# Performance work log

Hardware: AMD Instinct MI355X
Metric: run time of the kernel (lower is better)

Reference implementation:

```python
import jax, jax.numpy as jnp
import numpy as np
from jax import lax

B, C, H, W = 4, 256, 128, 128
K = 3
EPS = 1e-5
SLOPE = 0.01  # nn.LeakyReLU default

def rpad(x, p):
    return jnp.pad(x, ((0, 0), (0, 0), (p, p), (p, p)), mode='reflect')

def conv(x, w, groups=1):
    return lax.conv_general_dilated(x, w, (1, 1), 'VALID',
        dimension_numbers=('NCHW', 'OIHW', 'NCHW'), feature_group_count=groups)

def instance_norm(x):
    m = x.mean(axis=(2, 3), keepdims=True)
    v = x.var(axis=(2, 3), keepdims=True)
    return (x - m) * lax.rsqrt(v + EPS)

def kernel_predict(s, sw, sb, pw, pb, bw, bb):
    # s: [B, SC, K, K]; reflect-padded 'same' conv keeps KxK spatial
    ws = conv(rpad(s, (K - 1) // 2), sw) + sb[None, :, None, None]
    w_spatial = ws.reshape(s.shape[0], C, 1, K, K)   # n_groups == C -> in//groups == 1
    pooled = s.mean(axis=(2, 3))                     # AdaptiveAvgPool2d((1,1))
    w_point = pooled @ pw.reshape(C, -1).T + pb      # [B, C] (1x1 grouped, groups==C)
    bias = pooled @ bw.reshape(C, -1).T + bb         # [B, C]
    return w_spatial, w_point, bias

def ada_conv(x, w_spatial, w_point, bias, cw, cb):
    x = instance_norm(x)
    xp = rpad(x, (K - 1) // 2)
    dw = lambda xi, wi: conv(xi[None], wi, groups=C)[0]
    y = jax.vmap(dw)(xp, w_spatial)                  # per-sample dynamic depthwise conv
    # grouped 1x1 conv with groups == channels == per-channel scale + bias
    y = y * w_point[:, :, None, None] + bias[:, :, None, None]
    y = conv(rpad(y, 1), cw) + cb[None, :, None, None]  # shared 3x3 reflect conv
    return y

def lrelu(x):
    return jnp.where(x >= 0, x, SLOPE * x)

def upsample2(x):
    return jnp.repeat(jnp.repeat(x, 2, axis=2), 2, axis=3)  # nn.Upsample nearest x2

def avgpool2(x):
    b, c, h, w = x.shape
    return x.reshape(b, c, h // 2, 2, w // 2, 2).mean(axis=(3, 5))


def setup_inputs() -> dict:
    key = jax.random.key(0)
    ks = jax.random.split(key, 24)
    n = lambda k, shp, s=1.0: jax.random.normal(k, shp, dtype=jnp.float32) * s
    return {
        'c_hf': n(ks[0], (B, C, H, W)),
        'c_lf': n(ks[1], (B, C, H // 2, W // 2)),
        's_hf': n(ks[2], (B, C, K, K)),
        's_lf': n(ks[3], (B, C, K, K)),
        'h_sw': n(ks[4], (C, C, K, K), 0.05), 'h_sb': n(ks[5], (C,), 0.05),
        'h_pw': n(ks[6], (C, C, 1, 1), 0.05), 'h_pb': n(ks[7], (C,), 0.05),
        'h_bw': n(ks[8], (C, C, 1, 1), 0.05), 'h_bb': n(ks[9], (C,), 0.05),
        'l_sw': n(ks[10], (C, C, K, K), 0.05), 'l_sb': n(ks[11], (C,), 0.05),
        'l_pw': n(ks[12], (C, C, 1, 1), 0.05), 'l_pb': n(ks[13], (C,), 0.05),
        'l_bw': n(ks[14], (C, C, 1, 1), 0.05), 'l_bb': n(ks[15], (C,), 0.05),
        'ada_h_w': n(ks[16], (C, C, 3, 3), 0.05), 'ada_h_b': n(ks[17], (C,), 0.05),
        'ada_l_w': n(ks[18], (C, C, 3, 3), 0.05), 'ada_l_b': n(ks[19], (C,), 0.05),
        'h2h': n(ks[20], (C, C, 3, 3), 0.05),
        'l2h': n(ks[21], (C, C, 3, 3), 0.05),
        'h2l': n(ks[22], (C, C, 3, 3), 0.05),
        'l2l': n(ks[23], (C, C, 3, 3), 0.05),
    }


def reference(c_hf, c_lf, s_hf, s_lf,
              h_sw, h_sb, h_pw, h_pb, h_bw, h_bb,
              l_sw, l_sb, l_pw, l_pb, l_bw, l_bb,
              ada_h_w, ada_h_b, ada_l_w, ada_l_b,
              h2h, l2h, h2l, l2l):
    hws, hwp, hb = kernel_predict(s_hf, h_sw, h_sb, h_pw, h_pb, h_bw, h_bb)
    lws, lwp, lb = kernel_predict(s_lf, l_sw, l_sb, l_pw, l_pb, l_bw, l_bb)
    hf = lrelu(ada_conv(c_hf, hws, hwp, hb, ada_h_w, ada_h_b))
    lf = lrelu(ada_conv(c_lf, lws, lwp, lb, ada_l_w, ada_l_b))
    # OctConv 'normal', groups=1 (not depthwise): cross-frequency fusion
    hf_out = conv(rpad(hf, 1), h2h) + conv(rpad(upsample2(lf), 1), l2h)
    lf_out = conv(rpad(lf, 1), l2l) + conv(rpad(avgpool2(hf), 1), h2l)
    return lrelu(hf_out), lrelu(lf_out)
```

## Files before the change

### kernel.cpp

```cpp
#include <hip/hip_runtime.h>
#include <hip/hip_bf16.h>

#define CDIM 256
#define EPS 1e-5f
#define SLOPE 0.01f

using f32x4  = __attribute__((ext_vector_type(4))) float;
typedef __bf16 bf16x8 __attribute__((ext_vector_type(8)));
typedef unsigned short u16x8 __attribute__((ext_vector_type(8)));

enum : size_t {
  OFF_WS_HF   = 0,
  OFF_WS_LF   = 9216,
  OFF_WP_HF   = 20480,
  OFF_BS_HF   = 21504,
  OFF_WP_LF   = 22528,
  OFF_BS_LF   = 23552,
  OFF_MEAN_HF = 24576,
  OFF_RSTD_HF = 25600,
  OFF_MEAN_LF = 26624,
  OFF_RSTD_LF = 27648,
  OFF_U16     = 32768,
};
enum : size_t {
  U_YH  = 0,
  U_YL  = 16777216,
  U_HFA = 20971520,
  U_LFA = 37748736,
  U_HFP = 41943040,
  U_PK  = 46137344,
  PK_SZ = 589824,
  U_PKPH = U_PK + 6 * PK_SZ,
  PH_SZ  = 1048576,
  U_PHB  = U_PKPH + PH_SZ,
  U_END  = U_PHB + 16777216,
};
enum : size_t { TOTAL_F = OFF_U16 + (U_END + 1) / 2 };

__device__ float g_scratch[TOTAL_F];

__device__ __forceinline__ int refl(int q, int n) {
  return q < 0 ? -q : (q >= n ? 2 * n - 2 - q : q);
}
__device__ __forceinline__ float lrelu(float v) { return v >= 0.f ? v : SLOPE * v; }
__device__ __forceinline__ unsigned short f2bf(float f) {
  unsigned int u = __float_as_uint(f);
  u += 0x7fffu + ((u >> 16) & 1u);
  return (unsigned short)(u >> 16);
}
__device__ __forceinline__ float bf2f(unsigned short h) {
  return __uint_as_float(((unsigned int)h) << 16);
}
__device__ __forceinline__ void gload_lds16(const void* g, void* l) {
  __builtin_amdgcn_global_load_lds(
      (const __attribute__((address_space(1))) unsigned int*)g,
      (__attribute__((address_space(3))) unsigned int*)l, 16, 0, 0);
}

__global__ __launch_bounds__(256) void k_ws(const float* __restrict__ s_hf,
                                            const float* __restrict__ sw_hf,
                                            const float* __restrict__ sb_hf,
                                            float* __restrict__ ws_hf,
                                            const float* __restrict__ s_lf,
                                            const float* __restrict__ sw_lf,
                                            const float* __restrict__ sb_lf,
                                            float* __restrict__ ws_lf) {
  const bool lf = blockIdx.y != 0;
  const float* s  = lf ? s_lf : s_hf;
  const float* sw = lf ? sw_lf : sw_hf;
  const float* sb = lf ? sb_lf : sb_hf;
  float* ws_out   = lf ? ws_lf : ws_hf;
  int bo = blockIdx.x;
  int o = bo & (CDIM - 1);
  int c = threadIdx.x;
  int b = bo >> 8;
  float sv[9], wv[9];
  const float* sp = s + (size_t)(b * CDIM + c) * 9;
  const float* wp = sw + (size_t)(o * CDIM + c) * 9;
#pragma unroll
  for (int i = 0; i < 9; i++) { sv[i] = sp[i]; wv[i] = wp[i]; }
  float out9[9];
#pragma unroll
  for (int i = 0; i < 3; i++)
#pragma unroll
    for (int j = 0; j < 3; j++) {
      float a = 0.f;
#pragma unroll
      for (int dy = 0; dy < 3; dy++) {
        int u = i + dy - 1; u = (u < 0) ? 1 : (u > 2 ? 1 : u);
#pragma unroll
        for (int dx = 0; dx < 3; dx++) {
          int v = j + dx - 1; v = (v < 0) ? 1 : (v > 2 ? 1 : v);
          a += sv[u * 3 + v] * wv[dy * 3 + dx];
        }
      }
      out9[i * 3 + j] = a;
    }
  __shared__ float red[256 * 9];
#pragma unroll
  for (int i = 0; i < 9; i++) red[c * 9 + i] = out9[i];
  __syncthreads();
  for (int st = 128; st > 0; st >>= 1) {
    if (c < st)
#pragma unroll
      for (int i = 0; i < 9; i++) red[c * 9 + i] += red[(c + st) * 9 + i];
    __syncthreads();
  }
  if (c < 9) ws_out[(size_t)bo * 9 + c] = red[c] + sb[o];
}

__global__ __launch_bounds__(256) void k_point(const float* __restrict__ s_hf,
                                               const float* __restrict__ pw_hf,
                                               const float* __restrict__ pb_hf,
                                               const float* __restrict__ bw_hf,
                                               const float* __restrict__ bb_hf,
                                               float* __restrict__ wp_hf,
                                               float* __restrict__ bs_hf,
                                               const float* __restrict__ s_lf,
                                               const float* __restrict__ pw_lf,
                                               const float* __restrict__ pb_lf,
                                               const float* __restrict__ bw_lf,
                                               const float* __restrict__ bb_lf,
                                               float* __restrict__ wp_lf,
                                               float* __restrict__ bs_lf) {
  const bool lf = blockIdx.y != 0;
  const float* s  = lf ? s_lf : s_hf;
  const float* pw = lf ? pw_lf : pw_hf;
  const float* pb = lf ? pb_lf : pb_hf;
  const float* bw = lf ? bw_lf : bw_hf;
  const float* bb = lf ? bb_lf : bb_hf;
  float* wp_out = lf ? wp_lf : wp_hf;
  float* bs_out = lf ? bs_lf : bs_hf;
  int b = blockIdx.x, o = threadIdx.x;
  __shared__ float pl[CDIM];
  const float* sp = s + (size_t)(b * CDIM + o) * 9;
  float a9 = 0.f;
#pragma unroll
  for (int j = 0; j < 9; j++) a9 += sp[j];
  pl[o] = a9 * (1.f / 9.f);
  __syncthreads();
  float a = pb[o], d = bb[o];
  const float4* pw4 = (const float4*)(pw + (size_t)o * CDIM);
  const float4* bw4 = (const float4*)(bw + (size_t)o * CDIM);
  const float4* pl4 = (const float4*)pl;
  for (int c4 = 0; c4 < CDIM / 4; c4++) {
    float4 p = pl4[c4];
    float4 w1 = pw4[c4], w2 = bw4[c4];
    a += p.x * w1.x + p.y * w1.y + p.z * w1.z + p.w * w1.w;
    d += p.x * w2.x + p.y * w2.y + p.z * w2.z + p.w * w2.w;
  }
  wp_out[b * CDIM + o] = a;
  bs_out[b * CDIM + o] = d;
}

__global__ __launch_bounds__(256) void k_istats(const float* __restrict__ xh,
                                                float* __restrict__ mh, float* __restrict__ rh,
                                                const float* __restrict__ xl,
                                                float* __restrict__ ml, float* __restrict__ rl) {
  const bool lf = blockIdx.x >= 1024;
  int plane = lf ? blockIdx.x - 1024 : blockIdx.x;
  const float* x = lf ? xl : xh;
  float* mean = lf ? ml : mh;
  float* rstd = lf ? rl : rh;
  const int HW = lf ? 4096 : 16384;
  const float4* p = (const float4*)(x + (size_t)plane * HW);
  int n4 = HW >> 2;
  float s = 0.f, q = 0.f;
  for (int i = threadIdx.x; i < n4; i += 256) {
    float4 v = p[i];
    s += v.x + v.y + v.z + v.w;
    q += v.x * v.x + v.y * v.y + v.z * v.z + v.w * v.w;
  }
  __shared__ float rs[256], rq[256];
  rs[threadIdx.x] = s; rq[threadIdx.x] = q;
  __syncthreads();
  for (int st = 128; st > 0; st >>= 1) {
    if (threadIdx.x < st) {
      rs[threadIdx.x] += rs[threadIdx.x + st];
      rq[threadIdx.x] += rq[threadIdx.x + st];
    }
    __syncthreads();
  }
  if (threadIdx.x == 0) {
    float m = rs[0] / HW;
    float v = rq[0] / HW - m * m;
    mean[plane] = m;
    rstd[plane] = rsqrtf(v + EPS);
  }
}

__global__ void k_packall(const float* __restrict__ w_adah, const float* __restrict__ w_h2h,
                          const float* __restrict__ w_adal, const float* __restrict__ w_l2l,
                          const float* __restrict__ w_h2l, const float* __restrict__ w_l2h,
                          unsigned short* __restrict__ pk, unsigned short* __restrict__ pkph) {
  int seg = blockIdx.y;
  int i = blockIdx.x * 256 + threadIdx.x;
  if (seg < 5) {
    if (i >= 589824) return;
    const float* srcs[5] = {w_adah, w_h2h, w_adal, w_l2l, w_h2l};
    const int slot[5] = {0, 1, 3, 4, 5};
    const float* w = srcs[seg];
    int j = i & 7, l = (i >> 3) & 63, mf = (i >> 9) & 15, icc = (i >> 13) & 7, tap = i >> 16;
    int oc = mf * 16 + (l & 15);
    int ic = icc * 32 + (l >> 4) * 8 + j;
    pk[(size_t)slot[seg] * PK_SZ + i] = f2bf(w[((size_t)oc * 256 + ic) * 9 + tap]);
  } else {
    int j = i & 7, l = (i >> 3) & 63, mf = (i >> 9) & 15, icc = (i >> 13) & 7, tapph = i >> 16;
    int tap = tapph & 3, phase = tapph >> 2;
    int tx = tap & 1, ty = tap >> 1;
    int a = phase >> 1, bp = phase & 1;
    int oc = mf * 16 + (l & 15);
    int ic = icc * 32 + (l >> 4) * 8 + j;
    int ys = (a == 0) ? (ty == 0 ? 0 : 1) : (ty == 0 ? 0 : 2);
    int yc = (a == 0) ? (ty == 0 ? 1 : 2) : (ty == 0 ? 2 : 1);
    int xs = (bp == 0) ? (tx == 0 ? 0 : 1) : (tx == 0 ? 0 : 2);
    int xc = (bp == 0) ? (tx == 0 ? 1 : 2) : (tx == 0 ? 2 : 1);
    const float* wb = w_l2h + ((size_t)oc * 256 + ic) * 9;
    float acc = 0.f;
    for (int dy = ys; dy < ys + yc; dy++)
      for (int dx = xs; dx < xs + xc; dx++) acc += wb[dy * 3 + dx];
    pkph[i] = f2bf(acc);
  }
}

template <int LW>
__global__ __launch_bounds__(256) void k_dwt(const float* __restrict__ x,
                                             const float* __restrict__ ws,
                                             const float* __restrict__ mean,
                                             const float* __restrict__ rstd,
                                             const float* __restrict__ wp,
                                             const float* __restrict__ bs,
                                             unsigned short* __restrict__ out) {
  constexpr int W = 1 << LW, H = W, HW = W * W;
  int t = threadIdx.x;
  int xt = (LW > 6) ? (blockIdx.x & ((W >> 6) - 1)) : 0;
  int icb = (LW > 6) ? (blockIdx.x >> (LW - 6)) : blockIdx.x;
  int y = blockIdx.y, b = blockIdx.z;
  __shared__ unsigned short tr[64][66];
  const int xg = t & 15;
  const int chq = t >> 4;
  const int x0 = xt * 64 + xg * 4;
  const int sy0 = refl(y - 1, H), sy2 = refl(y + 1, H);
  const int xm = refl(x0 - 1, W);
  const int xq = refl(x0 + 4, W);
#pragma unroll
  for (int rr = 0; rr < 4; ++rr) {
    int icl = rr * 16 + chq;
    int plane = b * CDIM + icb * 64 + icl;
    const float* xpb = x + (size_t)plane * HW;
    float m = mean[plane], r = rstd[plane], sc = wp[plane], bi = bs[plane];
    const float* w9p = ws + (size_t)plane * 9;
    float w9[9];
#pragma unroll
    for (int i = 0; i < 9; i++) w9[i] = w9p[i];
    float sumw = w9[0] + w9[1] + w9[2] + w9[3] + w9[4] + w9[5] + w9[6] + w9[7] + w9[8];
    const float* r0 = xpb + sy0 * W;
    const float* r1 = xpb + y * W;
    const float* r2 = xpb + sy2 * W;
    float4 v0 = *(const float4*)(r0 + x0);
    float4 v1 = *(const float4*)(r1 + x0);
    float4 v2 = *(const float4*)(r2 + x0);
    float e0[6] = {r0[xm], v0.x, v0.y, v0.z, v0.w, r0[xq]};
    float e1[6] = {r1[xm], v1.x, v1.y, v1.z, v1.w, r1[xq]};
    float e2[6] = {r2[xm], v2.x, v2.y, v2.z, v2.w, r2[xq]};
    float mterm = m * sumw;
#pragma unroll
    for (int j = 0; j < 4; ++j) {
      float a = w9[0] * e0[j] + w9[1] * e0[j + 1] + w9[2] * e0[j + 2] +
                w9[3] * e1[j] + w9[4] * e1[j + 1] + w9[5] * e1[j + 2] +
                w9[6] * e2[j] + w9[7] * e2[j + 1] + w9[8] * e2[j + 2];
      a -= mterm;
      tr[icl][xg * 4 + j] = f2bf(a * r * sc + bi);
    }
  }
  __syncthreads();
#pragma unroll
  for (int it2 = 0; it2 < 2; ++it2) {
    int s2 = it2 * 256 + t;
    int xl2 = s2 >> 3;
    int cg = s2 & 7;
    u16x8 v;
#pragma unroll
    for (int j = 0; j < 8; j++) v[j] = tr[cg * 8 + j][xl2];
    *(u16x8*)&out[((size_t)((b * H + y) * W + xt * 64 + xl2)) * CDIM + icb * 64 + cg * 8] = v;
  }
}

__global__ __launch_bounds__(256) void k_pool_nhwc(const unsigned short* __restrict__ in,
                                                   unsigned short* __restrict__ out) {
  int i = blockIdx.x * 256 + threadIdx.x;
  int cg = i & 31;
  int p = i >> 5;
  int X = p & 63, Y = (p >> 6) & 63, b = p >> 12;
  const unsigned short* s =
      in + ((size_t)(b * 128 + 2 * Y) * 128 + 2 * X) * CDIM + cg * 8;
  u16x8 v0 = *(const u16x8*)(s);
  u16x8 v1 = *(const u16x8*)(s + CDIM);
  u16x8 v2 = *(const u16x8*)(s + 128 * CDIM);
  u16x8 v3 = *(const u16x8*)(s + 128 * CDIM + CDIM);
  u16x8 r;
#pragma unroll
  for (int j = 0; j < 8; j++)
    r[j] = f2bf(0.25f * (bf2f(v0[j]) + bf2f(v1[j]) + bf2f(v2[j]) + bf2f(v3[j])));
  *(u16x8*)(out + (size_t)p * CDIM + cg * 8) = r;
}

template <int LW, bool DUAL, bool UPSB, bool NCHWOUT, bool ACC>
__global__ __launch_bounds__(256, 2) void k_conv_mfma(
    const unsigned short* __restrict__ srcA, const unsigned short* __restrict__ srcB,
    const unsigned short* __restrict__ wpkA, const unsigned short* __restrict__ wpkB,
    const float* __restrict__ bias, const unsigned short* __restrict__ accsrc,
    void* __restrict__ outp) {
  constexpr int W = 1 << LW, H = W, HW = W * W;
  constexpr int ROWS = 256 >> LW;
  constexpr int R = ROWS + 2, Cw = W + 2;
  constexpr int RC = R * Cw;
  constexpr int RCPAD = (RC + 63) & ~63;
  constexpr int NIT = RCPAD / 64;
  __shared__ __align__(16) unsigned short tin[RCPAD * 32];
  __shared__ __align__(16) unsigned short wlds[9 * 4 * 64 * 8];

  const int t = threadIdx.x;
  const int l = t & 63, wv = t >> 6;
  const int l15 = l & 15, l4 = l >> 4;

  const int hwid = blockIdx.x;
  const int nwg = gridDim.x;
  const int wk = (hwid & 7) * (nwg >> 3) + (hwid >> 3);
  const int mb = wk & 3;
  const int pixbase = (wk >> 2) * 256;
  const int b = pixbase >> (2 * LW);
  const int y0 = (pixbase >> LW) & (H - 1);

  f32x4 acc[4][4];
#pragma unroll
  for (int mi = 0; mi < 4; mi++)
#pragma unroll
    for (int nf = 0; nf < 4; nf++) acc[mi][nf] = (f32x4){0.f, 0.f, 0.f, 0.f};

  const int nsrc = DUAL ? 2 : 1;
  for (int src = 0; src < nsrc; ++src) {
    const unsigned short* ysrc = src ? srcB : srcA;
    const unsigned short* wpk = src ? wpkB : wpkA;
    const bool ups = UPSB && (src == 1);

    const unsigned short* inptr[NIT];
#pragma unroll
    for (int it = 0; it < NIT; ++it) {
      int rc = it * 64 + (t >> 2);
      int rcc = rc < RC - 1 ? rc : RC - 1;
      int r = rcc / Cw, tc = rcc - r * Cw;
      int gy = refl(y0 - 1 + r, H);
      int gx = refl(tc - 1, W);
      int sy, sx, sw;
      if (ups) { sy = gy >> 1; sx = gx >> 1; sw = W >> 1; }
      else     { sy = gy;      sx = gx;      sw = W; }
      int gsrc = (t & 3) ^ (tc & 3);
      inptr[it] = ysrc + (((size_t)(b * sw + sy) * sw + sx) * CDIM + gsrc * 8);
    }
    const unsigned short* wsrc = wpk + ((size_t)(mb * 4 + wv) * 64 + l) * 8;

    for (int icc = 0; icc < 8; ++icc) {
      __syncthreads();
#pragma unroll
      for (int it = 0; it < NIT; ++it)
        gload_lds16(inptr[it] + icc * 32, &tin[(size_t)(it * 256 + t) * 8]);
#pragma unroll
      for (int tap = 0; tap < 9; ++tap)
        gload_lds16(wsrc + ((size_t)tap * 8 + (size_t)icc) * 8192,
                    &wlds[(size_t)(tap * 256 + t) * 8]);
      __syncthreads();

      __builtin_amdgcn_s_setprio(1);
#pragma unroll
      for (int tap = 0; tap < 9; ++tap) {
        const int dy = tap / 3, dx = tap - 3 * (tap / 3);
        bf16x8 af[4];
#pragma unroll
        for (int mi = 0; mi < 4; mi++)
          af[mi] = *(const bf16x8*)&wlds[(size_t)((tap * 4 + mi) * 64 + l) * 8];
#pragma unroll
        for (int nf = 0; nf < 4; nf++) {
          int pl = wv * 64 + nf * 16 + l15;
          int py = pl >> LW;
          int c = pl & (W - 1);
          int tcol = c + dx;
          int idx16 = ((py + dy) * Cw + tcol) * 4 + (l4 ^ (tcol & 3));
          bf16x8 bfv = *(const bf16x8*)&tin[(size_t)idx16 * 8];
#pragma unroll
          for (int mi = 0; mi < 4; mi++)
            acc[mi][nf] = __builtin_amdgcn_mfma_f32_16x16x32_bf16(af[mi], bfv, acc[mi][nf], 0, 0, 0);
        }
      }
      __builtin_amdgcn_s_setprio(0);
    }
  }

#pragma unroll
  for (int mi = 0; mi < 4; mi++) {
    int oc0 = mb * 64 + mi * 16 + l4 * 4;
    float bv[4];
#pragma unroll
    for (int rr = 0; rr < 4; rr++) bv[rr] = bias ? bias[oc0 + rr] : 0.f;
#pragma unroll
    for (int nf = 0; nf < 4; nf++) {
      int p = pixbase + wv * 64 + nf * 16 + l15;
      if (NCHWOUT) {
        float* o = (float*)outp;
        int pin = p & (HW - 1);
        int bb2 = p >> (2 * LW);
        int yy = pin >> LW, xx = pin & (W - 1);
        int ph = ((yy & 1) << 1) | (xx & 1);
        int q = (yy >> 1) * (W / 2) + (xx >> 1);
#pragma unroll
        for (int rr = 0; rr < 4; rr++) {
          float v = acc[mi][nf][rr] + bv[rr];
          if (ACC)
            v += bf2f(accsrc[((size_t)(bb2 * CDIM + oc0 + rr) * 4 + ph) * (HW / 4) + q]);
          o[((size_t)(bb2 * CDIM + oc0 + rr)) * HW + pin] = lrelu(v);
        }
      } else {
        unsigned short* o = (unsigned short*)outp;
        ushort4 pk;
        pk.x = f2bf(lrelu(acc[mi][nf][0] + bv[0]));
        pk.y = f2bf(lrelu(acc[mi][nf][1] + bv[1]));
        pk.z = f2bf(lrelu(acc[mi][nf][2] + bv[2]));
        pk.w = f2bf(lrelu(acc[mi][nf][3] + bv[3]));
        *(ushort4*)&o[(size_t)p * CDIM + oc0] = pk;
      }
    }
  }
}

__global__ __launch_bounds__(256, 3) void k_conv_up(
    const unsigned short* __restrict__ lf, const unsigned short* __restrict__ wph,
    unsigned short* __restrict__ phb) {
  constexpr int NIT = 5;
  __shared__ __align__(16) unsigned short tin[320 * 64 / 2];
  __shared__ __align__(16) unsigned short wlds[4 * 256 * 8];

  const int t = threadIdx.x;
  const int l = t & 63, wv = t >> 6;
  const int l15 = l & 15, l4 = l >> 4;

  const int hwid = blockIdx.x;
  const int wk = (hwid & 7) * 128 + (hwid >> 3);
  const int mb = wk & 3;
  const int phase = (wk >> 2) & 3;
  const int tile = (wk >> 4) & 15;
  const int b = wk >> 8;
  const int a = phase >> 1, bp = phase & 1;
  const int Y0 = tile * 4;

  f32x4 acc[4][4];
#pragma unroll
  for (int mi = 0; mi < 4; mi++)
#pragma unroll
    for (int nf = 0; nf < 4; nf++) acc[mi][nf] = (f32x4){0.f, 0.f, 0.f, 0.f};

  const unsigned short* inptr[NIT];
#pragma unroll
  for (int it = 0; it < NIT; ++it) {
    int s = it * 64 + (t >> 2);
    int row = s >> 6, col = s & 63;
    int ly = Y0 - 1 + a + row;
    ly = ly < 0 ? 0 : (ly > 63 ? 63 : ly);
    int gsrc = (t & 3) ^ (col & 3);
    inptr[it] = lf + (((size_t)(b * 64 + ly) * 64 + col) * CDIM + gsrc * 8);
  }
  const unsigned short* wsrc = wph + ((size_t)(mb * 4 + wv) * 64 + l) * 8;

  for (int icc = 0; icc < 8; ++icc) {
    __syncthreads();
#pragma unroll
    for (int it = 0; it < NIT; ++it)
      gload_lds16(inptr[it] + icc * 32, &tin[(size_t)(it * 256 + t) * 8]);
#pragma unroll
    for (int tap = 0; tap < 4; ++tap)
      gload_lds16(wsrc + ((size_t)(phase * 4 + tap) * 8 + (size_t)icc) * 8192,
                  &wlds[(size_t)(tap * 256 + t) * 8]);
    __syncthreads();

    __builtin_amdgcn_s_setprio(1);
#pragma unroll
    for (int tap = 0; tap < 4; ++tap) {
      const int ty = tap >> 1, tx = tap & 1;
      bf16x8 af[4];
#pragma unroll
      for (int mi = 0; mi < 4; mi++)
        af[mi] = *(const bf16x8*)&wlds[(size_t)((tap * 4 + mi) * 64 + l) * 8];
#pragma unroll
      for (int nf = 0; nf < 4; nf++) {
        int pl = wv * 64 + nf * 16 + l15;
        int py = pl >> 6;
        int col = pl & 63;
        int tcol = col - 1 + bp + tx;
        tcol = tcol < 0 ? 0 : (tcol > 63 ? 63 : tcol);
        int idx16 = ((py + ty) * 64 + tcol) * 4 + (l4 ^ (tcol & 3));
        bf16x8 bfv = *(const bf16x8*)&tin[(size_t)idx16 * 8];
#pragma unroll
        for (int mi = 0; mi < 4; mi++)
          acc[mi][nf] = __builtin_amdgcn_mfma_f32_16x16x32_bf16(af[mi], bfv, acc[mi][nf], 0, 0, 0);
      }
    }
    __builtin_amdgcn_s_setprio(0);
  }

#pragma unroll
  for (int mi = 0; mi < 4; mi++) {
    int oc0 = mb * 64 + mi * 16 + l4 * 4;
#pragma unroll
    for (int nf = 0; nf < 4; nf++) {
      int pl = wv * 64 + nf * 16 + l15;
      int py = pl >> 6, col = pl & 63;
      size_t base = ((size_t)(b * CDIM + oc0) * 4 + phase) * 4096 + (Y0 + py) * 64 + col;
#pragma unroll
      for (int rr = 0; rr < 4; rr++)
        phb[base + (size_t)rr * 4 * 4096] = f2bf(acc[mi][nf][rr]);
    }
  }
}

extern "C" void kernel_launch(void* const* d_in, const int* in_sizes, int n_in,
                              void* d_out, int out_size, void* d_ws, size_t ws_size,
                              hipStream_t stream) {
  (void)in_sizes; (void)n_in; (void)out_size;
  const float* c_hf = (const float*)d_in[0];
  const float* c_lf = (const float*)d_in[1];
  const float* s_hf = (const float*)d_in[2];
  const float* s_lf = (const float*)d_in[3];
  const float* h_sw = (const float*)d_in[4];
  const float* h_sb = (const float*)d_in[5];
  const float* h_pw = (const float*)d_in[6];
  const float* h_pb = (const float*)d_in[7];
  const float* h_bw = (const float*)d_in[8];
  const float* h_bb = (const float*)d_in[9];
  const float* l_sw = (const float*)d_in[10];
  const float* l_sb = (const float*)d_in[11];
  const float* l_pw = (const float*)d_in[12];
  const float* l_pb = (const float*)d_in[13];
  const float* l_bw = (const float*)d_in[14];
  const float* l_bb = (const float*)d_in[15];
  const float* ada_h_w = (const float*)d_in[16];
  const float* ada_h_b = (const float*)d_in[17];
  const float* ada_l_w = (const float*)d_in[18];
  const float* ada_l_b = (const float*)d_in[19];
  const float* h2h = (const float*)d_in[20];
  const float* l2h = (const float*)d_in[21];
  const float* h2l = (const float*)d_in[22];
  const float* l2l = (const float*)d_in[23];

  const int B = 4, H = 128, W = 128;

  float* base;
  size_t need = (size_t)TOTAL_F * sizeof(float);
  if (ws_size >= need) {
    base = (float*)d_ws;
  } else {
    void* p = nullptr;
    hipGetSymbolAddress(&p, HIP_SYMBOL(g_scratch));
    base = (float*)p;
  }

  float* ws_hf = base + OFF_WS_HF;
  float* ws_lf = base + OFF_WS_LF;
  float* wp_hf = base + OFF_WP_HF;
  float* bs_hf = base + OFF_BS_HF;
  float* wp_lf = base + OFF_WP_LF;
  float* bs_lf = base + OFF_BS_LF;
  float* mean_hf = base + OFF_MEAN_HF;
  float* rstd_hf = base + OFF_RSTD_HF;
  float* mean_lf = base + OFF_MEAN_LF;
  float* rstd_lf = base + OFF_RSTD_LF;
  unsigned short* u16 = (unsigned short*)(base + OFF_U16);
  unsigned short* yh = u16 + U_YH;
  unsigned short* yl = u16 + U_YL;
  unsigned short* hfA = u16 + U_HFA;
  unsigned short* lfA = u16 + U_LFA;
  unsigned short* hfP = u16 + U_HFP;
  unsigned short* pk      = u16 + U_PK;
  unsigned short* pk_adah = pk + 0 * PK_SZ;
  unsigned short* pk_h2h  = pk + 1 * PK_SZ;
  unsigned short* pk_adal = pk + 3 * PK_SZ;
  unsigned short* pk_l2l  = pk + 4 * PK_SZ;
  unsigned short* pk_h2l  = pk + 5 * PK_SZ;
  unsigned short* pk_ph   = u16 + U_PKPH;
  unsigned short* phb     = u16 + U_PHB;

  float* out_hf = (float*)d_out;
  float* out_lf = (float*)d_out + 16777216;

  k_packall<<<dim3(4096, 6), dim3(256), 0, stream>>>(ada_h_w, h2h, ada_l_w, l2l, h2l, l2h,
                                                     pk, pk_ph);

  k_ws<<<dim3(B * CDIM, 2), dim3(256), 0, stream>>>(s_hf, h_sw, h_sb, ws_hf,
                                                    s_lf, l_sw, l_sb, ws_lf);
  k_point<<<dim3(B, 2), dim3(256), 0, stream>>>(s_hf, h_pw, h_pb, h_bw, h_bb, wp_hf, bs_hf,
                                                s_lf, l_pw, l_pb, l_bw, l_bb, wp_lf, bs_lf);

  k_istats<<<dim3(2048), dim3(256), 0, stream>>>(c_hf, mean_hf, rstd_hf,
                                                 c_lf, mean_lf, rstd_lf);

  k_dwt<7><<<dim3(8, 128, 4), dim3(256), 0, stream>>>(c_hf, ws_hf, mean_hf, rstd_hf, wp_hf, bs_hf, yh);
  k_dwt<6><<<dim3(4, 64, 4), dim3(256), 0, stream>>>(c_lf, ws_lf, mean_lf, rstd_lf, wp_lf, bs_lf, yl);

  k_conv_mfma<7, false, false, false, false><<<dim3(1024), dim3(256), 0, stream>>>(
      yh, nullptr, pk_adah, nullptr, ada_h_b, nullptr, hfA);
  k_conv_mfma<6, false, false, false, false><<<dim3(256), dim3(256), 0, stream>>>(
      yl, nullptr, pk_adal, nullptr, ada_l_b, nullptr, lfA);

  k_conv_up<<<dim3(1024), dim3(256), 0, stream>>>(lfA, pk_ph, phb);

  k_pool_nhwc<<<dim3(2048), dim3(256), 0, stream>>>(hfA, hfP);

  k_conv_mfma<7, false, false, true, true><<<dim3(1024), dim3(256), 0, stream>>>(
      hfA, nullptr, pk_h2h, nullptr, nullptr, phb, out_hf);

  k_conv_mfma<6, true, false, true, false><<<dim3(256), dim3(256), 0, stream>>>(
      lfA, hfP, pk_l2l, pk_h2l, nullptr, nullptr, out_lf);
}
```

Baseline: 383.6 us.

## Add wide 512-thread implicit-GEMM conv kernel for high-frequency 3x3 convs

Adds a new k_conv_w kernel that uses 512-thread workgroups with 8 waves covering 128 output channels by 256 pixels per block. It double-buffers the input halo tile across input-channel chunks and reloads the weights per chunk. The two 128x128 high-frequency convolutions now use it, with half as many blocks as the previous k_conv_mfma. The larger tile is meant to improve weight and input reuse per block and to overlap loads with MFMA work, at the cost of more LDS and registers per block and lower occupancy.

```diff
diff --git a/kernel.cpp b/kernel.cpp
--- a/kernel.cpp
+++ b/kernel.cpp
@@ -432,6 +432,134 @@
   }
 }
 
+template <int LW, bool NCHWOUT, bool ACC>
+__global__ __launch_bounds__(512, 2) void k_conv_w(
+    const unsigned short* __restrict__ src, const unsigned short* __restrict__ wpk,
+    const float* __restrict__ bias, const unsigned short* __restrict__ accsrc,
+    void* __restrict__ outp) {
+  constexpr int W = 1 << LW, H = W, HW = W * W;
+  constexpr int ROWS = 256 >> LW;
+  constexpr int R = ROWS + 2, Cw = W + 2;
+  constexpr int RC = R * Cw;
+  constexpr int NIT = (RC + 127) / 128;
+  constexpr int RCPAD = NIT * 128;
+  __shared__ __align__(16) unsigned short tin[2][RCPAD * 32];
+  __shared__ __align__(16) unsigned short wlds[9 * 8 * 64 * 8];
+
+  const int t = threadIdx.x;
+  const int l = t & 63, wv = t >> 6;
+  const int og = wv >> 2, pq = wv & 3;
+  const int l15 = l & 15, l4 = l >> 4;
+
+  const int hwid = blockIdx.x;
+  const int nwg = gridDim.x;
+  const int wk = (hwid & 7) * (nwg >> 3) + (hwid >> 3);
+  const int mb = wk & 1;
+  const int pixbase = (wk >> 1) * 256;
+  const int b = pixbase >> (2 * LW);
+  const int y0 = (pixbase >> LW) & (H - 1);
+
+  f32x4 acc[4][4];
+#pragma unroll
+  for (int mi = 0; mi < 4; mi++)
+#pragma unroll
+    for (int nf = 0; nf < 4; nf++) acc[mi][nf] = (f32x4){0.f, 0.f, 0.f, 0.f};
+
+  const unsigned short* inptr[NIT];
+#pragma unroll
+  for (int it = 0; it < NIT; ++it) {
+    int rc = it * 128 + (t >> 2);
+    int rcc = rc < RC - 1 ? rc : RC - 1;
+    int r = rcc / Cw, tc = rcc - r * Cw;
+    int gy = refl(y0 - 1 + r, H);
+    int gx = refl(tc - 1, W);
+    int gsrc = (t & 3) ^ (tc & 3);
+    inptr[it] = src + (((size_t)(b * W + gy) * W + gx) * CDIM + gsrc * 8);
+  }
+  const unsigned short* wsrc = wpk + ((size_t)(mb * 8 + wv) * 64 + l) * 8;
+
+#pragma unroll
+  for (int it = 0; it < NIT; ++it)
+    gload_lds16(inptr[it], &tin[0][(size_t)(it * 512 + t) * 8]);
+
+#pragma unroll 1
+  for (int icc = 0; icc < 8; ++icc) {
+    const int buf = icc & 1;
+#pragma unroll
+    for (int tap = 0; tap < 9; ++tap)
+      gload_lds16(wsrc + ((size_t)tap * 8 + (size_t)icc) * 8192,
+                  &wlds[(size_t)(tap * 512 + t) * 8]);
+    if (icc < 7) {
+#pragma unroll
+      for (int it = 0; it < NIT; ++it)
+        gload_lds16(inptr[it] + (icc + 1) * 32, &tin[buf ^ 1][(size_t)(it * 512 + t) * 8]);
+      asm volatile("s_waitcnt vmcnt(%0)" ::"n"(NIT) : "memory");
+    } else {
+      asm volatile("s_waitcnt vmcnt(0)" ::: "memory");
+    }
+    __builtin_amdgcn_s_barrier();
+
+    __builtin_amdgcn_s_setprio(1);
+#pragma unroll
+    for (int tap = 0; tap < 9; ++tap) {
+      const int dy = tap / 3, dx = tap - 3 * (tap / 3);
+      bf16x8 af[4];
+#pragma unroll
+      for (int mi = 0; mi < 4; mi++)
+        af[mi] = *(const bf16x8*)&wlds[(size_t)((tap * 8 + og * 4 + mi) * 64 + l) * 8];
+#pragma unroll
+      for (int nf = 0; nf < 4; nf++) {
+        int pl = pq * 64 + nf * 16 + l15;
+        int py = pl >> LW;
+        int c = pl & (W - 1);
+        int tcol = c + dx;
+        int idx16 = ((py + dy) * Cw + tcol) * 4 + (l4 ^ (tcol & 3));
+        bf16x8 bfv = *(const bf16x8*)&tin[buf][(size_t)idx16 * 8];
+#pragma unroll
+        for (int mi = 0; mi < 4; mi++)
+          acc[mi][nf] = __builtin_amdgcn_mfma_f32_16x16x32_bf16(af[mi], bfv, acc[mi][nf], 0, 0, 0);
+      }
+    }
+    __builtin_amdgcn_s_setprio(0);
+    __builtin_amdgcn_s_barrier();
+  }
+
+#pragma unroll
+  for (int mi = 0; mi < 4; mi++) {
+    int oc0 = mb * 128 + og * 64 + mi * 16 + l4 * 4;
+    float bv[4];
+#pragma unroll
+    for (int rr = 0; rr < 4; rr++) bv[rr] = bias ? bias[oc0 + rr] : 0.f;
+#pragma unroll
+    for (int nf = 0; nf < 4; nf++) {
+      int p = pixbase + pq * 64 + nf * 16 + l15;
+      if (NCHWOUT) {
+        float* o = (float*)outp;
+        int pin = p & (HW - 1);
+        int bb2 = p >> (2 * LW);
+        int yy = pin >> LW, xx = pin & (W - 1);
+        int ph = ((yy & 1) << 1) | (xx & 1);
+        int q = (yy >> 1) * (W / 2) + (xx >> 1);
+#pragma unroll
+        for (int rr = 0; rr < 4; rr++) {
+          float v = acc[mi][nf][rr] + bv[rr];
+          if (ACC)
+            v += bf2f(accsrc[((size_t)(bb2 * CDIM + oc0 + rr) * 4 + ph) * (HW / 4) + q]);
+          o[((size_t)(bb2 * CDIM + oc0 + rr)) * HW + pin] = lrelu(v);
+        }
+      } else {
+        unsigned short* o = (unsigned short*)outp;
+        ushort4 pk;
+        pk.x = f2bf(lrelu(acc[mi][nf][0] + bv[0]));
+        pk.y = f2bf(lrelu(acc[mi][nf][1] + bv[1]));
+        pk.z = f2bf(lrelu(acc[mi][nf][2] + bv[2]));
+        pk.w = f2bf(lrelu(acc[mi][nf][3] + bv[3]));
+        *(ushort4*)&o[(size_t)p * CDIM + oc0] = pk;
+      }
+    }
+  }
+}
+
 __global__ __launch_bounds__(256, 3) void k_conv_up(
     const unsigned short* __restrict__ lf, const unsigned short* __restrict__ wph,
     unsigned short* __restrict__ phb) {
@@ -604,8 +732,8 @@
   k_dwt<7><<<dim3(8, 128, 4), dim3(256), 0, stream>>>(c_hf, ws_hf, mean_hf, rstd_hf, wp_hf, bs_hf, yh);
   k_dwt<6><<<dim3(4, 64, 4), dim3(256), 0, stream>>>(c_lf, ws_lf, mean_lf, rstd_lf, wp_lf, bs_lf, yl);
 
-  k_conv_mfma<7, false, false, false, false><<<dim3(1024), dim3(256), 0, stream>>>(
-      yh, nullptr, pk_adah, nullptr, ada_h_b, nullptr, hfA);
+  k_conv_w<7, false, false><<<dim3(512), dim3(512), 0, stream>>>(
+      yh, pk_adah, ada_h_b, nullptr, hfA);
   k_conv_mfma<6, false, false, false, false><<<dim3(256), dim3(256), 0, stream>>>(
       yl, nullptr, pk_adal, nullptr, ada_l_b, nullptr, lfA);
 
@@ -613,8 +741,8 @@
 
   k_pool_nhwc<<<dim3(2048), dim3(256), 0, stream>>>(hfA, hfP);
 
-  k_conv_mfma<7, false, false, true, true><<<dim3(1024), dim3(256), 0, stream>>>(
-      hfA, nullptr, pk_h2h, nullptr, nullptr, phb, out_hf);
+  k_conv_w<7, true, true><<<dim3(512), dim3(512), 0, stream>>>(
+      hfA, pk_h2h, nullptr, phb, out_hf);
 
   k_conv_mfma<6, true, false, true, false><<<dim3(256), dim3(256), 0, stream>>>(
       lfA, hfP, pk_l2l, pk_h2l, nullptr, nullptr, out_lf);
```

Measured after the change: 396.1 us. +3.3%, slower.
